# Performance work log

Measured on AMD Instinct MI355X. Metric: run time of the kernel, lower is better.

## Reference

```python
import jax, jax.numpy as jnp
import numpy as np

B, D, N, C = 2048, 128, 100000, 100
T = 2.0


def setup_inputs() -> dict:
    key = jax.random.key(0)
    k1, k2, k3 = jax.random.split(key, 3)
    x = jax.random.normal(k1, (B, D), dtype=jnp.float32)
    Address = jax.random.normal(k2, (N, D), dtype=jnp.float32)
    M = jax.random.uniform(k3, (N, C), dtype=jnp.float32)
    return {"x": x, "Address": Address, "M": M}


def reference(x, Address, M):
    # dist[b,n] = ||x_b - A_n||_2 via the expanded quadratic form (same as torch mm+norms)
    sq = (-2.0 * (x @ Address.T)
          + jnp.sum(Address * Address, axis=1)[None, :]
          + jnp.sum(x * x, axis=1)[:, None])
    dist = jnp.sqrt(jnp.maximum(sq, 0.0))  # clamp guards fp roundoff negatives
    # softmin over addresses == softmax(-dist/T)
    soft_w = jax.nn.softmax(-dist / T, axis=1)  # (B, N)
    logits = soft_w @ M  # (B, n_classes)
    return logits
```

## Files before the change

### kernel.cpp

```cpp
#include <hip/hip_runtime.h>

#define NTOT 100000
#define BD 128
#define NC 100
#define CP 112
#define NS 32
#define BROWS 2048
#define LOG2E 1.4426950408889634f

typedef short short8 __attribute__((ext_vector_type(8)));
typedef float f32x4 __attribute__((ext_vector_type(4)));

__device__ __forceinline__ unsigned short f2bf(float f) {
    union { float f; unsigned u; } v; v.f = f;
    unsigned r = v.u + 0x7FFFu + ((v.u >> 16) & 1u);
    return (unsigned short)(r >> 16);
}

__device__ __forceinline__ unsigned pkbf(float a, float b) {
    unsigned r;
    asm("v_cvt_pk_bf16_f32 %0, %1, %2" : "=v"(r) : "v"(a), "v"(b));
    return r;
}

__device__ __forceinline__ float rawsqrt(float x) {
    float r;
    asm("v_sqrt_f32 %0, %1" : "=v"(r) : "v"(x));
    return r;
}

__device__ __forceinline__ float rawexp2(float x) {
    float r;
    asm("v_exp_f32 %0, %1" : "=v"(r) : "v"(x));
    return r;
}

__device__ __forceinline__ void gload16(const void* g, void* l) {
    __builtin_amdgcn_global_load_lds((const __attribute__((address_space(1))) void*)g,
                                     (__attribute__((address_space(3))) void*)l, 16, 0, 0);
}

__global__ __launch_bounds__(256) void prep_A(const float* __restrict__ A,
                                              unsigned short* __restrict__ Abf,
                                              float* __restrict__ anorm) {
    const int tid = threadIdx.x;
    const int row = blockIdx.x * 16 + (tid >> 4);
    const int g = tid & 15;
    const float* src = A + (size_t)row * BD + g * 8;
    float4 v0 = *(const float4*)src, v1 = *(const float4*)(src + 4);
    uint4 u;
    u.x = pkbf(v0.x, v0.y); u.y = pkbf(v0.z, v0.w);
    u.z = pkbf(v1.x, v1.y); u.w = pkbf(v1.z, v1.w);
    float ss = v0.x*v0.x + v0.y*v0.y + v0.z*v0.z + v0.w*v0.w
             + v1.x*v1.x + v1.y*v1.y + v1.z*v1.z + v1.w*v1.w;
    ss += __shfl_xor(ss, 1); ss += __shfl_xor(ss, 2);
    ss += __shfl_xor(ss, 4); ss += __shfl_xor(ss, 8);
    *(uint4*)((char*)Abf + (size_t)row * 256 + ((g * 16) ^ ((row & 15) << 4))) = u;
    if (g == 0) anorm[row] = ss;
}

__global__ __launch_bounds__(256) void prep_M(const float* __restrict__ M,
                                              unsigned short* __restrict__ Mt) {
    __shared__ unsigned short lm[100 * 264];
    const int t = threadIdx.x;
    const int n0 = blockIdx.x * 256;
    const int rows = min(256, NTOT - n0);
    const float4* Mf4 = (const float4*)(M + (size_t)n0 * NC);
    #pragma unroll
    for (int k = 0; k < 25; ++k) {
        int f = k * 256 + t;
        if (f < rows * 25) {
            int row = (int)(((unsigned)f * 5243u) >> 17);
            int c4 = f - row * 25;
            float4 v = Mf4[f];
            lm[(c4 * 4 + 0) * 264 + row] = f2bf(v.x);
            lm[(c4 * 4 + 1) * 264 + row] = f2bf(v.y);
            lm[(c4 * 4 + 2) * 264 + row] = f2bf(v.z);
            lm[(c4 * 4 + 3) * 264 + row] = f2bf(v.w);
        }
    }
    __syncthreads();
    if (n0 + t < NTOT) {
        for (int c = 0; c < NC; ++c)
            Mt[(size_t)c * NTOT + n0 + t] = lm[c * 264 + t];
        #pragma unroll
        for (int z = NC; z < CP; ++z)
            Mt[(size_t)z * NTOT + n0 + t] = 0;
    }
}

__global__ __launch_bounds__(256, 2) void fused_main(
    const float* __restrict__ x, const unsigned short* __restrict__ Abf,
    const float* __restrict__ anorm, const unsigned short* __restrict__ Mt,
    float* __restrict__ pO, float* __restrict__ pL)
{
    __shared__ __align__(16) unsigned short a_lds[2][4096];
    __shared__ __align__(16) unsigned short m_lds[2][3584];
    __shared__ __align__(16) unsigned short p_lds[8][640];

    const int tid = threadIdx.x, wave = tid >> 6, lane = tid & 63;
    const int l15 = lane & 15, lhi = lane >> 4;
    const int bid = blockIdx.x;
    const int chunk = bid & (NS - 1), rg = bid >> 5;
    const int ts = chunk * 97 + (chunk < 21 ? chunk : 21);
    const int tiles = (chunk < 21) ? 98 : 97;
    const int n0c = ts * 32;
    const int qbw = rg * 128 + wave * 32;

    short8 qf[2][4];
    float nx[2];
    #pragma unroll
    for (int t = 0; t < 2; ++t) {
        float s = 0.f;
        #pragma unroll
        for (int kk = 0; kk < 4; ++kk) {
            const float* xp = x + (size_t)(qbw + t * 16 + l15) * BD + kk * 32 + lhi * 8;
            float4 v0 = *(const float4*)xp, v1 = *(const float4*)(xp + 4);
            uint4 uu;
            uu.x = pkbf(v0.x, v0.y); uu.y = pkbf(v0.z, v0.w);
            uu.z = pkbf(v1.x, v1.y); uu.w = pkbf(v1.z, v1.w);
            qf[t][kk] = *(short8*)&uu;
            s += v0.x*v0.x + v0.y*v0.y + v0.z*v0.z + v0.w*v0.w
               + v1.x*v1.x + v1.y*v1.y + v1.z*v1.z + v1.w*v1.w;
        }
        s += __shfl_xor(s, 16); s += __shfl_xor(s, 32);
        nx[t] = s;
    }

    const char* aFix = (const char*)Abf + tid * 16;
    const int r0 = tid >> 2, sg0 = ((tid & 3) - r0 - (r0 >> 2)) & 3;
    const char* mFix0 = (const char*)Mt + (size_t)r0 * (NTOT * 2) + sg0 * 16;
    const int L1 = tid + 256, r1 = L1 >> 2, sg1 = ((L1 & 3) - r1 - (r1 >> 2)) & 3;
    const char* mFix1 = (const char*)Mt + (size_t)r1 * (NTOT * 2) + sg1 * 16;

    auto stage = [&](int buf, int t) {
        const int n0 = n0c + t * 32;
        const char* ab = aFix + (size_t)n0 * 256;
        char* al = (char*)&a_lds[buf][0] + tid * 16;
        gload16(ab, al);
        gload16(ab + 4096, al + 4096);
        gload16(mFix0 + (size_t)n0 * 2, (char*)&m_lds[buf][0] + tid * 16);
        if (tid < 192)
            gload16(mFix1 + (size_t)n0 * 2, (char*)&m_lds[buf][0] + (tid + 256) * 16);
    };

    f32x4 Oacc[2][7];
    const f32x4 zf = {0.f, 0.f, 0.f, 0.f};
    #pragma unroll
    for (int t = 0; t < 2; ++t)
        #pragma unroll
        for (int c0 = 0; c0 < 7; ++c0) Oacc[t][c0] = zf;
    float lsum[2] = {0.f, 0.f};

    stage(0, 0);
    __syncthreads();

    for (int it = 0; it < tiles; ++it) {
        const int buf = it & 1;
        const int n0 = n0c + it * 32;
        if (it + 1 < tiles) stage(buf ^ 1, it + 1);

        float an[8];
        #pragma unroll
        for (int j = 0; j < 8; ++j)
            an[j] = anorm[n0 + (j >> 2) * 16 + lhi * 4 + (j & 3)];

        f32x4 s0[2], s1[2];
        s0[0] = zf; s0[1] = zf; s1[0] = zf; s1[1] = zf;
        const char* ab = (const char*)&a_lds[buf][0];
        #pragma unroll
        for (int kk = 0; kk < 4; ++kk) {
            const int sw = (kk * 64 + lhi * 16) ^ (l15 << 4);
            short8 b0 = *(const short8*)(ab + l15 * 256 + sw);
            short8 b1 = *(const short8*)(ab + (16 + l15) * 256 + sw);
            s0[0] = __builtin_amdgcn_mfma_f32_16x16x32_bf16(b0, qf[0][kk], s0[0], 0, 0, 0);
            s1[0] = __builtin_amdgcn_mfma_f32_16x16x32_bf16(b1, qf[0][kk], s1[0], 0, 0, 0);
            s0[1] = __builtin_amdgcn_mfma_f32_16x16x32_bf16(b0, qf[1][kk], s0[1], 0, 0, 0);
            s1[1] = __builtin_amdgcn_mfma_f32_16x16x32_bf16(b1, qf[1][kk], s1[1], 0, 0, 0);
        }

        #pragma unroll
        for (int t = 0; t < 2; ++t) {
            float p[8];
            #pragma unroll
            for (int j = 0; j < 8; ++j) {
                float sv = (j < 4) ? s0[t][j & 3] : s1[t][j & 3];
                float sq = fmaf(sv, -2.f, an[j]) + nx[t];
                float d = rawsqrt(fmaxf(sq, 0.f));
                float pv = rawexp2(d * (-0.5f * LOG2E));
                p[j] = pv;
                lsum[t] += pv;
            }
            char* pw = (char*)&p_lds[wave * 2 + t][0] + l15 * 80 + lhi * 8;
            uint2 w0 = { pkbf(p[0], p[1]), pkbf(p[2], p[3]) };
            uint2 w1 = { pkbf(p[4], p[5]), pkbf(p[6], p[7]) };
            *(uint2*)(pw) = w0;
            *(uint2*)(pw + 32) = w1;
        }

        const short8 pa0 = *(const short8*)((const char*)&p_lds[wave * 2 + 0][0] + l15 * 80 + lhi * 16);
        const short8 pa1 = *(const short8*)((const char*)&p_lds[wave * 2 + 1][0] + l15 * 80 + lhi * 16);
        const char* mb = (const char*)&m_lds[buf][0];
        #pragma unroll
        for (int c0 = 0; c0 < 7; ++c0) {
            const int c = c0 * 16 + l15;
            short8 bm = *(const short8*)(mb + c * 64 + (((lhi + c + (c >> 2)) & 3) * 16));
            Oacc[0][c0] = __builtin_amdgcn_mfma_f32_16x16x32_bf16(pa0, bm, Oacc[0][c0], 0, 0, 0);
            Oacc[1][c0] = __builtin_amdgcn_mfma_f32_16x16x32_bf16(pa1, bm, Oacc[1][c0], 0, 0, 0);
        }

        __syncthreads();
    }

    const size_t crow = (size_t)chunk * BROWS;
    #pragma unroll
    for (int t = 0; t < 2; ++t) {
        float ls = lsum[t];
        ls += __shfl_xor(ls, 16); ls += __shfl_xor(ls, 32);
        #pragma unroll
        for (int c0 = 0; c0 < 7; ++c0)
            #pragma unroll
            for (int r2 = 0; r2 < 4; ++r2)
                pO[(crow + qbw + t * 16 + lhi * 4 + r2) * CP + c0 * 16 + l15] = Oacc[t][c0][r2];
        if (lane < 16) pL[crow + qbw + t * 16 + lane] = ls;
    }
}

__global__ __launch_bounds__(128) void combine(
    const float* __restrict__ pO, const float* __restrict__ pL,
    float* __restrict__ out)
{
    const int r = blockIdx.x, c = threadIdx.x;
    if (c >= NC) return;
    float acc = 0.f, l = 0.f;
    #pragma unroll
    for (int i = 0; i < NS; ++i) {
        acc += pO[((size_t)i * BROWS + r) * CP + c];
        l   += pL[(size_t)i * BROWS + r];
    }
    out[(size_t)r * NC + c] = acc / l;
}

#define FBNS 16
#define FBCH 6250
#define KV 32
#define AST 136
#define MST 40
#define PST 40

__global__ __launch_bounds__(256, 2) void fused_fb(
    const float* __restrict__ x, const float* __restrict__ A,
    const float* __restrict__ M, float* __restrict__ pO,
    float* __restrict__ pM, float* __restrict__ pL)
{
    __shared__ __align__(16) unsigned short a_lds[KV * AST];
    __shared__ __align__(16) unsigned short mt_lds[CP * MST];
    __shared__ __align__(16) unsigned short p_lds[4][16 * PST];
    __shared__ float anorm_s[KV];

    const int tid  = threadIdx.x;
    const int wave = tid >> 6, lane = tid & 63;
    const int l15  = lane & 15, lhi = lane >> 4;
    const int bid  = blockIdx.x;
    const int chunk = bid & (FBNS - 1);
    const int rg    = bid >> 4;
    const int n0c   = chunk * FBCH;
    const int n1c   = n0c + FBCH;
    const int qbase = rg * 64 + wave * 16;
    const int q     = qbase + l15;

    short8 qf[4];
    float sumsq = 0.f;
    #pragma unroll
    for (int kk = 0; kk < 4; ++kk) {
        const float* xp = x + (size_t)q * BD + kk * 32 + lhi * 8;
        float4 v0 = *(const float4*)xp;
        float4 v1 = *(const float4*)(xp + 4);
        short8 f;
        f[0] = (short)f2bf(v0.x); f[1] = (short)f2bf(v0.y);
        f[2] = (short)f2bf(v0.z); f[3] = (short)f2bf(v0.w);
        f[4] = (short)f2bf(v1.x); f[5] = (short)f2bf(v1.y);
        f[6] = (short)f2bf(v1.z); f[7] = (short)f2bf(v1.w);
        qf[kk] = f;
        sumsq += v0.x*v0.x + v0.y*v0.y + v0.z*v0.z + v0.w*v0.w
               + v1.x*v1.x + v1.y*v1.y + v1.z*v1.z + v1.w*v1.w;
    }
    sumsq += __shfl_xor(sumsq, 16);
    sumsq += __shfl_xor(sumsq, 32);
    float nxr[4];
    #pragma unroll
    for (int r2 = 0; r2 < 4; ++r2) nxr[r2] = __shfl(sumsq, lhi * 4 + r2);

    const f32x4 zf = {0.f, 0.f, 0.f, 0.f};
    f32x4 Oacc[7];
    #pragma unroll
    for (int c = 0; c < 7; ++c) Oacc[c] = zf;
    float mrow[4] = {-1e30f, -1e30f, -1e30f, -1e30f};
    float lrow[4] = {0.f, 0.f, 0.f, 0.f};

    for (int n0 = n0c; n0 < n1c; n0 += KV) {
        __syncthreads();
        {
            int arow = tid >> 3, seg = tid & 7;
            int n = n0 + arow;
            float s2 = 0.f;
            unsigned short* dst = &a_lds[arow * AST + seg * 16];
            if (n < n1c) {
                const float* src = A + (size_t)n * BD + seg * 16;
                #pragma unroll
                for (int j = 0; j < 4; ++j) {
                    float4 v = ((const float4*)src)[j];
                    dst[j*4+0] = f2bf(v.x); dst[j*4+1] = f2bf(v.y);
                    dst[j*4+2] = f2bf(v.z); dst[j*4+3] = f2bf(v.w);
                    s2 += v.x*v.x + v.y*v.y + v.z*v.z + v.w*v.w;
                }
            } else {
                #pragma unroll
                for (int j = 0; j < 16; ++j) dst[j] = 0;
            }
            s2 += __shfl_xor(s2, 1);
            s2 += __shfl_xor(s2, 2);
            s2 += __shfl_xor(s2, 4);
            if (seg == 0) anorm_s[arow] = (n < n1c) ? s2 : 1e18f;
        }
        #pragma unroll
        for (int it = 0; it < 14; ++it) {
            int idx = tid + it * 256;
            int r2 = idx / CP;
            int c  = idx - r2 * CP;
            int n  = n0 + r2;
            float v = (c < NC && n < n1c) ? M[(size_t)n * NC + c] : 0.f;
            mt_lds[c * MST + r2] = f2bf(v);
        }
        __syncthreads();

        f32x4 s[2]; s[0] = zf; s[1] = zf;
        #pragma unroll
        for (int t = 0; t < 2; ++t) {
            #pragma unroll
            for (int kk = 0; kk < 4; ++kk) {
                short8 bf = *(const short8*)&a_lds[(t*16 + l15) * AST + kk*32 + lhi*8];
                s[t] = __builtin_amdgcn_mfma_f32_16x16x32_bf16(qf[kk], bf, s[t], 0, 0, 0);
            }
        }
        float na0 = anorm_s[l15], na1 = anorm_s[16 + l15];

        float pv0[4], pv1[4], fr[4];
        #pragma unroll
        for (int r2 = 0; r2 < 4; ++r2) {
            float s0 = nxr[r2] + na0 - 2.f * s[0][r2];
            float s1 = nxr[r2] + na1 - 2.f * s[1][r2];
            s0 = -0.5f * sqrtf(fmaxf(s0, 0.f));
            s1 = -0.5f * sqrtf(fmaxf(s1, 0.f));
            float v = fmaxf(s0, s1);
            v = fmaxf(v, __shfl_xor(v, 1));
            v = fmaxf(v, __shfl_xor(v, 2));
            v = fmaxf(v, __shfl_xor(v, 4));
            v = fmaxf(v, __shfl_xor(v, 8));
            float mnew = fmaxf(mrow[r2], v);
            float f = exp2f((mrow[r2] - mnew) * LOG2E);
            mrow[r2] = mnew;
            float p0 = exp2f((s0 - mnew) * LOG2E);
            float p1 = exp2f((s1 - mnew) * LOG2E);
            pv0[r2] = p0; pv1[r2] = p1;
            float ps = p0 + p1;
            ps += __shfl_xor(ps, 1);
            ps += __shfl_xor(ps, 2);
            ps += __shfl_xor(ps, 4);
            ps += __shfl_xor(ps, 8);
            lrow[r2] = lrow[r2] * f + ps;
            fr[r2] = f;
        }
        #pragma unroll
        for (int c = 0; c < 7; ++c)
            #pragma unroll
            for (int r2 = 0; r2 < 4; ++r2) Oacc[c][r2] *= fr[r2];

        #pragma unroll
        for (int r2 = 0; r2 < 4; ++r2) {
            p_lds[wave][(lhi*4 + r2) * PST +  0 + l15] = f2bf(pv0[r2]);
            p_lds[wave][(lhi*4 + r2) * PST + 16 + l15] = f2bf(pv1[r2]);
        }
        short8 pa = *(const short8*)&p_lds[wave][l15 * PST + lhi * 8];
        #pragma unroll
        for (int c = 0; c < 7; ++c) {
            short8 bm = *(const short8*)&mt_lds[(c*16 + l15) * MST + lhi * 8];
            Oacc[c] = __builtin_amdgcn_mfma_f32_16x16x32_bf16(pa, bm, Oacc[c], 0, 0, 0);
        }
    }

    const size_t crow = (size_t)chunk * 2048;
    #pragma unroll
    for (int c = 0; c < 7; ++c) {
        #pragma unroll
        for (int r2 = 0; r2 < 4; ++r2) {
            int row = qbase + lhi * 4 + r2;
            pO[(crow + row) * CP + c * 16 + l15] = Oacc[c][r2];
        }
    }
    if (l15 == 0) {
        #pragma unroll
        for (int r2 = 0; r2 < 4; ++r2) {
            int row = qbase + lhi * 4 + r2;
            pM[crow + row] = mrow[r2];
            pL[crow + row] = lrow[r2];
        }
    }
}

__global__ __launch_bounds__(128) void combine_fb(
    const float* __restrict__ pO, const float* __restrict__ pM,
    const float* __restrict__ pL, float* __restrict__ out)
{
    int r = blockIdx.x;
    int c = threadIdx.x;
    float mi[FBNS];
    float mg = -1e30f;
    #pragma unroll
    for (int i = 0; i < FBNS; ++i) { mi[i] = pM[i * 2048 + r]; mg = fmaxf(mg, mi[i]); }
    float w[FBNS];
    float lg = 0.f;
    #pragma unroll
    for (int i = 0; i < FBNS; ++i) {
        w[i] = exp2f((mi[i] - mg) * LOG2E);
        lg += pL[i * 2048 + r] * w[i];
    }
    if (c < NC) {
        float acc = 0.f;
        #pragma unroll
        for (int i = 0; i < FBNS; ++i)
            acc += pO[((size_t)i * 2048 + r) * CP + c] * w[i];
        out[(size_t)r * NC + c] = acc / lg;
    }
}

extern "C" void kernel_launch(void* const* d_in, const int* in_sizes, int n_in,
                              void* d_out, int out_size, void* d_ws, size_t ws_size,
                              hipStream_t stream) {
    const float* x = (const float*)d_in[0];
    const float* A = (const float*)d_in[1];
    const float* M = (const float*)d_in[2];
    float* out = (float*)d_out;

    const size_t FULL = 78022272;
    if (ws_size >= FULL) {
        unsigned short* Abf = (unsigned short*)d_ws;
        float* anorm = (float*)(Abf + (size_t)NTOT * BD);
        unsigned short* Mt = (unsigned short*)(anorm + NTOT);
        float* pO = (float*)(Mt + (size_t)CP * NTOT);
        float* pL = pO + (size_t)NS * BROWS * CP;
        prep_A<<<6250, 256, 0, stream>>>(A, Abf, anorm);
        prep_M<<<391, 256, 0, stream>>>(M, Mt);
        fused_main<<<512, 256, 0, stream>>>(x, Abf, anorm, Mt, pO, pL);
        combine<<<2048, 128, 0, stream>>>(pO, pL, out);
    } else {
        float* pO = (float*)d_ws;
        float* pM = pO + (size_t)FBNS * 2048 * CP;
        float* pL = pM + (size_t)FBNS * 2048;
        fused_fb<<<512, 256, 0, stream>>>(x, A, M, pO, pM, pL);
        combine_fb<<<2048, 128, 0, stream>>>(pO, pM, pL, out);
    }
}
```

Baseline: 282.8 us.

## Split key range into 64 chunks when workspace allows; vectorize prep_M stores

The main fused kernel now takes its chunk count and tile split as runtime parameters. When the workspace is large enough it launches 1024 blocks over 64 key chunks instead of 512 over 32, so more blocks can be resident on the GPU's many CUs. prep_M now writes the transposed bf16 M with 16-byte vector stores instead of scalar 2-byte stores. The cost is more partial-result traffic: the combine kernel has to read twice as many partials, and its loop is no longer unrolled.

```diff
diff --git a/kernel.cpp b/kernel.cpp
--- a/kernel.cpp
+++ b/kernel.cpp
@@ -4,7 +4,6 @@
 #define BD 128
 #define NC 100
 #define CP 112
-#define NS 32
 #define BROWS 2048
 #define LOG2E 1.4426950408889634f
 
@@ -61,7 +60,7 @@
 
 __global__ __launch_bounds__(256) void prep_M(const float* __restrict__ M,
                                               unsigned short* __restrict__ Mt) {
-    __shared__ unsigned short lm[100 * 264];
+    __shared__ __align__(16) unsigned short lm[100 * 264];
     const int t = threadIdx.x;
     const int n0 = blockIdx.x * 256;
     const int rows = min(256, NTOT - n0);
@@ -80,19 +79,25 @@
         }
     }
     __syncthreads();
-    if (n0 + t < NTOT) {
-        for (int c = 0; c < NC; ++c)
-            Mt[(size_t)c * NTOT + n0 + t] = lm[c * 264 + t];
-        #pragma unroll
-        for (int z = NC; z < CP; ++z)
-            Mt[(size_t)z * NTOT + n0 + t] = 0;
+    uint4* Mt4 = (uint4*)Mt;
+    const int nb = rows >> 3;
+    #pragma unroll
+    for (int k = 0; k < 14; ++k) {
+        int f = k * 256 + t;
+        int c = f >> 5, nblk = f & 31;
+        if (nblk < nb) {
+            uint4 v = {0u, 0u, 0u, 0u};
+            if (c < NC) v = *(const uint4*)&lm[c * 264 + nblk * 8];
+            Mt4[(size_t)c * (NTOT / 8) + (n0 >> 3) + nblk] = v;
+        }
     }
 }
 
 __global__ __launch_bounds__(256, 2) void fused_main(
     const float* __restrict__ x, const unsigned short* __restrict__ Abf,
     const float* __restrict__ anorm, const unsigned short* __restrict__ Mt,
-    float* __restrict__ pO, float* __restrict__ pL)
+    float* __restrict__ pO, float* __restrict__ pL,
+    int cmask, int cshift, int qq, int rr)
 {
     __shared__ __align__(16) unsigned short a_lds[2][4096];
     __shared__ __align__(16) unsigned short m_lds[2][3584];
@@ -101,9 +106,9 @@
     const int tid = threadIdx.x, wave = tid >> 6, lane = tid & 63;
     const int l15 = lane & 15, lhi = lane >> 4;
     const int bid = blockIdx.x;
-    const int chunk = bid & (NS - 1), rg = bid >> 5;
-    const int ts = chunk * 97 + (chunk < 21 ? chunk : 21);
-    const int tiles = (chunk < 21) ? 98 : 97;
+    const int chunk = bid & cmask, rg = bid >> cshift;
+    const int ts = chunk * qq + (chunk < rr ? chunk : rr);
+    const int tiles = (chunk < rr) ? qq + 1 : qq;
     const int n0c = ts * 32;
     const int qbw = rg * 128 + wave * 32;
 
@@ -228,13 +233,12 @@
 
 __global__ __launch_bounds__(128) void combine(
     const float* __restrict__ pO, const float* __restrict__ pL,
-    float* __restrict__ out)
+    float* __restrict__ out, int nch)
 {
     const int r = blockIdx.x, c = threadIdx.x;
     if (c >= NC) return;
     float acc = 0.f, l = 0.f;
-    #pragma unroll
-    for (int i = 0; i < NS; ++i) {
+    for (int i = 0; i < nch; ++i) {
         acc += pO[((size_t)i * BROWS + r) * CP + c];
         l   += pL[(size_t)i * BROWS + r];
     }
@@ -442,17 +446,25 @@
     const float* M = (const float*)d_in[2];
     float* out = (float*)d_out;
 
-    const size_t FULL = 78022272;
-    if (ws_size >= FULL) {
+    const size_t BASE = 25600000 + 400000 + 22400000;
+    const size_t NEED64 = BASE + (size_t)64 * BROWS * CP * 4 + (size_t)64 * BROWS * 4;
+    const size_t NEED32 = BASE + (size_t)32 * BROWS * CP * 4 + (size_t)32 * BROWS * 4;
+
+    if (ws_size >= NEED32) {
         unsigned short* Abf = (unsigned short*)d_ws;
         float* anorm = (float*)(Abf + (size_t)NTOT * BD);
         unsigned short* Mt = (unsigned short*)(anorm + NTOT);
         float* pO = (float*)(Mt + (size_t)CP * NTOT);
-        float* pL = pO + (size_t)NS * BROWS * CP;
+        const int nch = (ws_size >= NEED64) ? 64 : 32;
+        float* pL = pO + (size_t)nch * BROWS * CP;
         prep_A<<<6250, 256, 0, stream>>>(A, Abf, anorm);
         prep_M<<<391, 256, 0, stream>>>(M, Mt);
-        fused_main<<<512, 256, 0, stream>>>(x, Abf, anorm, Mt, pO, pL);
-        combine<<<2048, 128, 0, stream>>>(pO, pL, out);
+        if (nch == 64) {
+            fused_main<<<1024, 256, 0, stream>>>(x, Abf, anorm, Mt, pO, pL, 63, 6, 48, 53);
+        } else {
+            fused_main<<<512, 256, 0, stream>>>(x, Abf, anorm, Mt, pO, pL, 31, 5, 97, 21);
+        }
+        combine<<<2048, 128, 0, stream>>>(pO, pL, out, nch);
     } else {
         float* pO = (float*)d_ws;
         float* pM = pO + (size_t)FBNS * 2048 * CP;
```

Result: no change. 287.9 us (+1.8%).
